# Performance work log

Measured on AMD Instinct MI355X. Metric: run time of the kernel, lower is better.

Reference implementation:

```python
import jax, jax.numpy as jnp
import numpy as np

N = 50000        # atoms
NEIGH = 12       # neighbors per atom
HID = 128
B = 500          # crystals (100 atoms each, contiguous)
NCLS = 2
BSTEPS, BMIN, BMAX = 40, 0.0, 8.0
ASTEPS, AMIN, AMAX = 10, -1.0, 1.0


def gbf(d, dmin, dmax, steps):
    # Gaussian basis expansion: exp(-(d - mu)^2 / gamma^2)
    filters = jnp.linspace(dmin, dmax, steps)
    gamma = (dmax - dmin) / steps
    return jnp.exp(-(d[..., None] - filters) ** 2 / gamma ** 2)


def sage_conv(x, W_l, b_l, W_r, dst, n):
    # PyG SAGEConv (mean aggr): out[d] = lin_l(mean_{src->d} x[src]) + lin_r(x[d])
    # lin commutes with mean, so project first (N x HID) to avoid a 600k x F gather.
    h = x @ W_l.T                                  # [N, HID]
    h_src = jnp.repeat(h, NEIGH, axis=0)           # source of edge e = e // NEIGH
    s = jax.ops.segment_sum(h_src, dst, num_segments=n)
    cnt = jax.ops.segment_sum(jnp.ones(dst.shape, h.dtype), dst, num_segments=n)
    agg = s / jnp.maximum(cnt, 1.0)[:, None]
    return agg + b_l + x @ W_r.T


def setup_inputs() -> dict:
    key = jax.random.key(0)
    ks = jax.random.split(key, 20)
    inp = {
        "bond_fea": jax.random.uniform(ks[0], (N, NEIGH), jnp.float32) * 8.0,
        "angle_fea": jax.random.uniform(ks[1], (N, NEIGH, NEIGH), jnp.float32) * 2.0 - 1.0,
        "species": jax.random.randint(ks[2], (N,), 0, 100),
        "nbr_idx": jax.random.randint(ks[3], (N, NEIGH), 0, N),
        "crys_idx": jnp.stack([jnp.arange(B) * 100, (jnp.arange(B) + 1) * 100], axis=1),
    }
    def w(k, shape):
        return jax.random.normal(k, shape, jnp.float32) * 0.05
    inp.update({
        "W1b": w(ks[4], (HID, BSTEPS * NEIGH)), "b1b": jnp.zeros((HID,), jnp.float32),
        "W1br": w(ks[5], (HID, BSTEPS * NEIGH)),
        "W1a": w(ks[6], (HID, ASTEPS * NEIGH * NEIGH)), "b1a": jnp.zeros((HID,), jnp.float32),
        "W1ar": w(ks[7], (HID, ASTEPS * NEIGH * NEIGH)),
        "W2b": w(ks[8], (HID, HID)), "b2b": jnp.zeros((HID,), jnp.float32),
        "W2br": w(ks[9], (HID, HID)),
        "W2a": w(ks[10], (HID, HID)), "b2a": jnp.zeros((HID,), jnp.float32),
        "W2ar": w(ks[11], (HID, HID)),
        "Wfc": w(ks[12], (NCLS, 2 * HID)), "bfc": jnp.zeros((NCLS,), jnp.float32),
    })
    return inp


def reference(bond_fea, angle_fea, W1b, b1b, W1br, W1a, b1a, W1ar,
              W2b, b2b, W2br, W2a, b2a, W2ar, Wfc, bfc,
              species, nbr_idx, crys_idx):
    dst = nbr_idx.reshape(-1)                               # [N*NEIGH]
    edge_fea = gbf(bond_fea, BMIN, BMAX, BSTEPS).reshape(N, -1)    # [N, 480]
    angle_f = gbf(angle_fea, AMIN, AMAX, ASTEPS).reshape(N, -1)    # [N, 1440]

    bo = jax.nn.relu(sage_conv(edge_fea, W1b, b1b, W1br, dst, N))
    ao = jax.nn.relu(sage_conv(angle_f, W1a, b1a, W1ar, dst, N))
    # dropout omitted (deterministic eval-mode reference)
    bo = jax.nn.relu(sage_conv(bo, W2b, b2b, W2br, dst, N))
    ao = jax.nn.relu(sage_conv(ao, W2a, b2a, W2ar, dst, N))

    crys_fea = jnp.concatenate([bo, ao], axis=1)            # [N, 256]
    # segment-mean pooling over contiguous [start, end) crystal ranges
    seg = jnp.searchsorted(crys_idx[:, 1], jnp.arange(N), side="right")
    cnt = (crys_idx[:, 1] - crys_idx[:, 0]).astype(crys_fea.dtype)
    pooled = jax.ops.segment_sum(crys_fea, seg, num_segments=B) / cnt[:, None]
    return pooled @ Wfc.T + bfc
```

## Files before the change

kernel.cpp:

```cpp
#include <hip/hip_runtime.h>

#define NEIGHB 12
#define HIDD 128
#define CAP 40

typedef _Float16 half8 __attribute__((ext_vector_type(8)));
typedef float f32x4 __attribute__((ext_vector_type(4)));

__global__ __launch_bounds__(256) void cvt_all(
    const float* __restrict__ W1b, const float* __restrict__ W1br, _Float16* __restrict__ O1b,
    const float* __restrict__ W1a, const float* __restrict__ W1ar, _Float16* __restrict__ O1a,
    const float* __restrict__ W2b, const float* __restrict__ W2br, _Float16* __restrict__ O2b,
    const float* __restrict__ W2a, const float* __restrict__ W2ar, _Float16* __restrict__ O2a) {
    int blk = blockIdx.x;
    const float *Wl, *Wr; _Float16* out; int K, Kp, base;
    if (blk < 512)       { Wl = W1b; Wr = W1br; out = O1b; K = 480;  Kp = 512;  base = 0; }
    else if (blk < 1984) { Wl = W1a; Wr = W1ar; out = O1a; K = 1440; Kp = 1472; base = 512; }
    else if (blk < 2112) { Wl = W2b; Wr = W2br; out = O2b; K = 128;  Kp = 128;  base = 1984; }
    else                 { Wl = W2a; Wr = W2ar; out = O2a; K = 128;  Kp = 128;  base = 2112; }
    int idx = (blk - base) * 256 + threadIdx.x;
    int n = idx / Kp, k = idx - n * Kp;
    float v = 0.f;
    if (k < K) v = (n < HIDD) ? Wl[(size_t)n * K + k] : Wr[(size_t)(n - HIDD) * K + k];
    out[idx] = (_Float16)v;
}

template <int MODE, int KTOT, int KP>
__global__ __launch_bounds__(256) void gemm_f16(
    const void* __restrict__ Ain, const _Float16* __restrict__ Wt,
    _Float16* __restrict__ Cl, _Float16* __restrict__ Cr, int rows) {
    constexpr int SUB  = (MODE == 2) ? 10 : 40;
    constexpr int RAWC = (MODE == 2) ? 144 : 12;
    constexpr float MU0 = (MODE == 2) ? -1.0f : 0.0f;
    constexpr float DMU = (MODE == 2) ? (2.0f / 9.0f) : (8.0f / 39.0f);

    __shared__ __align__(16) _Float16 As[64 * 64];
    __shared__ __align__(16) _Float16 Bs[256 * 64];

    const int tid = threadIdx.x;
    const int lane = tid & 63;
    const int wave = tid >> 6;
    const int iBase = blockIdx.x * 64;

    f32x4 acc[4][4];
#pragma unroll
    for (int a = 0; a < 4; ++a)
#pragma unroll
        for (int b = 0; b < 4; ++b)
#pragma unroll
            for (int r = 0; r < 4; ++r) acc[a][b][r] = 0.f;

    for (int kc = 0; kc < KP; kc += 64) {
        __syncthreads();
#pragma unroll
        for (int q = 0; q < 2; ++q) {
            int idx = tid + 256 * q;
            int m = idx >> 3, g = idx & 7;
            int gi = min(iBase + m, rows - 1);
            half8 v;
            if (MODE == 0) {
                v = *reinterpret_cast<const half8*>((const _Float16*)Ain + (size_t)gi * KP + kc + g * 8);
            } else {
                int k0 = kc + g * 8;
                if (k0 < KTOT) {
                    int j0 = k0 / SUB, t0 = k0 - j0 * SUB;
                    const float* rr = (const float*)Ain + (size_t)gi * RAWC;
                    float r0 = rr[j0];
                    float r1 = (MODE == 2 && t0 + 7 >= SUB) ? rr[min(j0 + 1, RAWC - 1)] : r0;
#pragma unroll
                    for (int e2 = 0; e2 < 8; ++e2) {
                        int t = t0 + e2;
                        bool c2 = (t >= SUB);
                        float d = (c2 ? r1 : r0) - (MU0 + (float)(c2 ? t - SUB : t) * DMU);
                        v[e2] = (_Float16)__expf(-25.f * d * d);
                    }
                } else {
#pragma unroll
                    for (int e2 = 0; e2 < 8; ++e2) v[e2] = (_Float16)0.f;
                }
            }
            *reinterpret_cast<half8*>(As + m * 64 + ((g ^ (m & 7)) << 3)) = v;
        }
#pragma unroll
        for (int q = 0; q < 8; ++q) {
            int idx = tid + 256 * q;
            int n = idx >> 3, g = idx & 7;
            half8 v = *reinterpret_cast<const half8*>(Wt + (size_t)n * KP + kc + g * 8);
            *reinterpret_cast<half8*>(Bs + n * 64 + ((g ^ (n & 7)) << 3)) = v;
        }
        __syncthreads();
#pragma unroll
        for (int s = 0; s < 2; ++s) {
            int cg = s * 4 + (lane >> 4);
            half8 af[4], bf[4];
#pragma unroll
            for (int a = 0; a < 4; ++a) {
                int m = a * 16 + (lane & 15);
                af[a] = *reinterpret_cast<const half8*>(As + m * 64 + ((cg ^ (m & 7)) << 3));
            }
#pragma unroll
            for (int b = 0; b < 4; ++b) {
                int n = wave * 64 + b * 16 + (lane & 15);
                bf[b] = *reinterpret_cast<const half8*>(Bs + n * 64 + ((cg ^ (n & 7)) << 3));
            }
#pragma unroll
            for (int a = 0; a < 4; ++a)
#pragma unroll
                for (int b = 0; b < 4; ++b)
                    acc[a][b] = __builtin_amdgcn_mfma_f32_16x16x32_f16(af[a], bf[b], acc[a][b], 0, 0, 0);
        }
    }

    _Float16* Cout = (wave < 2) ? Cl : Cr;
    int nBase = (wave & 1) * 64;
#pragma unroll
    for (int a = 0; a < 4; ++a) {
        int mrel = a * 16 + ((lane >> 4) << 2);
#pragma unroll
        for (int r = 0; r < 4; ++r) {
            int m = iBase + mrel + r;
            if (m < rows) {
#pragma unroll
                for (int b = 0; b < 4; ++b) {
                    int n = nBase + b * 16 + (lane & 15);
                    Cout[(size_t)m * HIDD + n] = (_Float16)acc[a][b][r];
                }
            }
        }
    }
}

__global__ void build_inc(const int* __restrict__ nbr, int* __restrict__ cnt,
                          int* __restrict__ inc, int nEdges) {
    int e = blockIdx.x * blockDim.x + threadIdx.x;
    if (e >= nEdges) return;
    int d = nbr[e];
    int src = e / NEIGHB;
    int pos = atomicAdd(&cnt[d], 1);
    if (pos < CAP) inc[(size_t)d * CAP + pos] = src;
}

__global__ __launch_bounds__(256) void agg_relu(
    const _Float16* __restrict__ Hl, const _Float16* __restrict__ Hr,
    const int* __restrict__ cnt, const int* __restrict__ inc,
    const float* __restrict__ bias, _Float16* __restrict__ O, int N) {
    int d = blockIdx.x * 16 + (threadIdx.x >> 4);
    if (d >= N) return;
    int c8 = (threadIdx.x & 15) * 8;
    int c = cnt[d];
    int cc = min(c, CAP);
    const int* lst = inc + (size_t)d * CAP;
    float s[8];
#pragma unroll
    for (int j = 0; j < 8; ++j) s[j] = 0.f;
    int e = 0;
    for (; e + 2 <= cc; e += 2) {
        int i0 = lst[e], i1 = lst[e + 1];
        half8 v0 = *reinterpret_cast<const half8*>(Hl + (size_t)i0 * HIDD + c8);
        half8 v1 = *reinterpret_cast<const half8*>(Hl + (size_t)i1 * HIDD + c8);
#pragma unroll
        for (int j = 0; j < 8; ++j) s[j] += (float)v0[j] + (float)v1[j];
    }
    if (e < cc) {
        half8 v0 = *reinterpret_cast<const half8*>(Hl + (size_t)lst[e] * HIDD + c8);
#pragma unroll
        for (int j = 0; j < 8; ++j) s[j] += (float)v0[j];
    }
    float inv = 1.f / (float)max(c, 1);
    half8 hr = *reinterpret_cast<const half8*>(Hr + (size_t)d * HIDD + c8);
    float4 b0 = *reinterpret_cast<const float4*>(bias + c8);
    float4 b1 = *reinterpret_cast<const float4*>(bias + c8 + 4);
    float bb[8] = {b0.x, b0.y, b0.z, b0.w, b1.x, b1.y, b1.z, b1.w};
    half8 o;
#pragma unroll
    for (int j = 0; j < 8; ++j)
        o[j] = (_Float16)fmaxf(s[j] * inv + bb[j] + (float)hr[j], 0.f);
    *reinterpret_cast<half8*>(O + (size_t)d * HIDD + c8) = o;
}

__global__ __launch_bounds__(256) void pool_fc(const _Float16* __restrict__ bo,
                                               const _Float16* __restrict__ ao,
                                               const int* __restrict__ crys,
                                               const float* __restrict__ Wfc,
                                               const float* __restrict__ bfc,
                                               float* __restrict__ out) {
    __shared__ float red0[256];
    __shared__ float red1[256];
    int b = blockIdx.x;
    int t = threadIdx.x;
    int s0 = crys[b * 2 + 0];
    int s1 = crys[b * 2 + 1];
    const _Float16* src = (t < HIDD) ? bo : ao;
    int col = t & (HIDD - 1);
    float s = 0.f;
    for (int i = s0; i < s1; ++i) s += (float)src[(size_t)i * HIDD + col];
    float pooled = s / (float)(s1 - s0);
    red0[t] = pooled * Wfc[t];
    red1[t] = pooled * Wfc[256 + t];
    __syncthreads();
    for (int off = 128; off >= 1; off >>= 1) {
        if (t < off) {
            red0[t] += red0[t + off];
            red1[t] += red1[t + off];
        }
        __syncthreads();
    }
    if (t == 0) {
        out[b * 2 + 0] = red0[0] + bfc[0];
        out[b * 2 + 1] = red1[0] + bfc[1];
    }
}

extern "C" void kernel_launch(void* const* d_in, const int* in_sizes, int n_in,
                              void* d_out, int out_size, void* d_ws, size_t ws_size,
                              hipStream_t stream) {
    const float* bond = (const float*)d_in[0];
    const float* angle = (const float*)d_in[1];
    const int* nbr = (const int*)d_in[3];
    const int* crys = (const int*)d_in[4];
    const float* W1b = (const float*)d_in[5];
    const float* b1b = (const float*)d_in[6];
    const float* W1br = (const float*)d_in[7];
    const float* W1a = (const float*)d_in[8];
    const float* b1a = (const float*)d_in[9];
    const float* W1ar = (const float*)d_in[10];
    const float* W2b = (const float*)d_in[11];
    const float* b2b = (const float*)d_in[12];
    const float* W2br = (const float*)d_in[13];
    const float* W2a = (const float*)d_in[14];
    const float* b2a = (const float*)d_in[15];
    const float* W2ar = (const float*)d_in[16];
    const float* Wfc = (const float*)d_in[17];
    const float* bfc = (const float*)d_in[18];
    float* out = (float*)d_out;

    const int N = in_sizes[2];
    const int B = in_sizes[4] / 2;
    const int nEdges = N * NEIGHB;

    char* p = (char*)d_ws;
    _Float16* Hl  = (_Float16*)p;  p += (size_t)N * HIDD * 2;
    _Float16* Hr  = (_Float16*)p;  p += (size_t)N * HIDD * 2;
    _Float16* bo  = (_Float16*)p;  p += (size_t)N * HIDD * 2;
    _Float16* ao  = (_Float16*)p;  p += (size_t)N * HIDD * 2;
    _Float16* bo2 = (_Float16*)p;  p += (size_t)N * HIDD * 2;
    _Float16* ao2 = (_Float16*)p;  p += (size_t)N * HIDD * 2;
    int* cnt = (int*)p;            p += (size_t)N * 4;
    int* inc = (int*)p;            p += (size_t)N * CAP * 4;
    _Float16* W1bp = (_Float16*)p; p += 256 * 512 * 2;
    _Float16* W1ap = (_Float16*)p; p += 256 * 1472 * 2;
    _Float16* W2bp = (_Float16*)p; p += 256 * 128 * 2;
    _Float16* W2ap = (_Float16*)p;

    hipMemsetAsync(cnt, 0, (size_t)N * 4, stream);
    build_inc<<<(nEdges + 255) / 256, 256, 0, stream>>>(nbr, cnt, inc, nEdges);
    cvt_all<<<2240, 256, 0, stream>>>(W1b, W1br, W1bp, W1a, W1ar, W1ap,
                                      W2b, W2br, W2bp, W2a, W2ar, W2ap);

    const int gB = (N + 63) / 64;
    const int aB = (N + 15) / 16;

    gemm_f16<1, 480, 512><<<gB, 256, 0, stream>>>(bond, W1bp, Hl, Hr, N);
    agg_relu<<<aB, 256, 0, stream>>>(Hl, Hr, cnt, inc, b1b, bo, N);
    gemm_f16<2, 1440, 1472><<<gB, 256, 0, stream>>>(angle, W1ap, Hl, Hr, N);
    agg_relu<<<aB, 256, 0, stream>>>(Hl, Hr, cnt, inc, b1a, ao, N);
    gemm_f16<0, 128, 128><<<gB, 256, 0, stream>>>(bo, W2bp, Hl, Hr, N);
    agg_relu<<<aB, 256, 0, stream>>>(Hl, Hr, cnt, inc, b2b, bo2, N);
    gemm_f16<0, 128, 128><<<gB, 256, 0, stream>>>(ao, W2ap, Hl, Hr, N);
    agg_relu<<<aB, 256, 0, stream>>>(Hl, Hr, cnt, inc, b2a, ao2, N);

    pool_fc<<<B, 256, 0, stream>>>(bo2, ao2, crys, Wfc, bfc, out);
}
```

Before: 431.3 us.

## Stage raw GBF inputs in LDS, split angle GEMM across N, widen gather unroll

For the fused Gaussian-expansion GEMMs, each block first copies its 64 rows of raw bond or angle values into shared memory with vectorized loads. The per-k-chunk expansion then reads from LDS instead of re-reading scattered global floats. The angle GEMM gains an N-split template parameter so two blocks each compute half the 256 output columns, doubling the grid. This adds parallelism but recomputes the expensive exp expansion twice per row tile. The aggregation kernel now loads four neighbor indices at once with an int4 and sums four gathered rows per iteration to raise memory-level parallelism.

```diff
diff --git a/kernel.cpp b/kernel.cpp
--- a/kernel.cpp
+++ b/kernel.cpp
@@ -25,28 +25,58 @@
     out[idx] = (_Float16)v;
 }
 
-template <int MODE, int KTOT, int KP>
+template <int MODE, int KTOT, int KP, int NS>
 __global__ __launch_bounds__(256) void gemm_f16(
     const void* __restrict__ Ain, const _Float16* __restrict__ Wt,
     _Float16* __restrict__ Cl, _Float16* __restrict__ Cr, int rows) {
     constexpr int SUB  = (MODE == 2) ? 10 : 40;
     constexpr int RAWC = (MODE == 2) ? 144 : 12;
+    constexpr int RST  = (MODE == 2) ? 148 : 12;
     constexpr float MU0 = (MODE == 2) ? -1.0f : 0.0f;
     constexpr float DMU = (MODE == 2) ? (2.0f / 9.0f) : (8.0f / 39.0f);
+    constexpr int BN = 256 / NS;
+    constexpr int NB = BN / 64;
 
     __shared__ __align__(16) _Float16 As[64 * 64];
-    __shared__ __align__(16) _Float16 Bs[256 * 64];
+    __shared__ __align__(16) _Float16 Bs[BN * 64];
+    __shared__ __align__(16) float rawS[(MODE != 0) ? 64 * RST : 4];
 
     const int tid = threadIdx.x;
     const int lane = tid & 63;
     const int wave = tid >> 6;
-    const int iBase = blockIdx.x * 64;
-
-    f32x4 acc[4][4];
+    const int nHalf = (NS == 2) ? ((int)blockIdx.x & 1) : 0;
+    const int mb = (NS == 2) ? ((int)blockIdx.x >> 1) : (int)blockIdx.x;
+    const int iBase = mb * 64;
+
+    if (MODE != 0) {
+        if (iBase + 64 <= rows) {
+            const float* gsrc = (const float*)Ain + (size_t)iBase * RAWC;
+            constexpr int NV4 = 64 * RAWC / 4;
+#pragma unroll
+            for (int q = 0; q < (NV4 + 255) / 256; ++q) {
+                int idx = tid + 256 * q;
+                if (NV4 % 256 == 0 || idx < NV4) {
+                    int r = idx / (RAWC / 4);
+                    int c4 = idx - r * (RAWC / 4);
+                    float4 v = *reinterpret_cast<const float4*>(gsrc + (size_t)idx * 4);
+                    *reinterpret_cast<float4*>(&rawS[r * RST + c4 * 4]) = v;
+                }
+            }
+        } else {
+            for (int idx = tid; idx < 64 * RAWC; idx += 256) {
+                int r = idx / RAWC, c = idx - r * RAWC;
+                int gi = iBase + r;
+                rawS[r * RST + c] = (gi < rows) ? ((const float*)Ain)[(size_t)gi * RAWC + c] : 0.f;
+            }
+        }
+        __syncthreads();
+    }
+
+    f32x4 acc[4][NB];
 #pragma unroll
     for (int a = 0; a < 4; ++a)
 #pragma unroll
-        for (int b = 0; b < 4; ++b)
+        for (int b = 0; b < NB; ++b)
 #pragma unroll
             for (int r = 0; r < 4; ++r) acc[a][b][r] = 0.f;
 
@@ -56,17 +86,16 @@
         for (int q = 0; q < 2; ++q) {
             int idx = tid + 256 * q;
             int m = idx >> 3, g = idx & 7;
-            int gi = min(iBase + m, rows - 1);
             half8 v;
             if (MODE == 0) {
+                int gi = min(iBase + m, rows - 1);
                 v = *reinterpret_cast<const half8*>((const _Float16*)Ain + (size_t)gi * KP + kc + g * 8);
             } else {
                 int k0 = kc + g * 8;
                 if (k0 < KTOT) {
                     int j0 = k0 / SUB, t0 = k0 - j0 * SUB;
-                    const float* rr = (const float*)Ain + (size_t)gi * RAWC;
-                    float r0 = rr[j0];
-                    float r1 = (MODE == 2 && t0 + 7 >= SUB) ? rr[min(j0 + 1, RAWC - 1)] : r0;
+                    float r0 = rawS[m * RST + j0];
+                    float r1 = (MODE == 2 && t0 + 7 >= SUB) ? rawS[m * RST + j0 + 1] : r0;
 #pragma unroll
                     for (int e2 = 0; e2 < 8; ++e2) {
                         int t = t0 + e2;
@@ -82,37 +111,36 @@
             *reinterpret_cast<half8*>(As + m * 64 + ((g ^ (m & 7)) << 3)) = v;
         }
 #pragma unroll
-        for (int q = 0; q < 8; ++q) {
+        for (int q = 0; q < BN / 32; ++q) {
             int idx = tid + 256 * q;
             int n = idx >> 3, g = idx & 7;
-            half8 v = *reinterpret_cast<const half8*>(Wt + (size_t)n * KP + kc + g * 8);
+            half8 v = *reinterpret_cast<const half8*>(
+                Wt + (size_t)(nHalf * BN + n) * KP + kc + g * 8);
             *reinterpret_cast<half8*>(Bs + n * 64 + ((g ^ (n & 7)) << 3)) = v;
         }
         __syncthreads();
 #pragma unroll
         for (int s = 0; s < 2; ++s) {
             int cg = s * 4 + (lane >> 4);
-            half8 af[4], bf[4];
+            half8 af[4], bf[NB];
 #pragma unroll
             for (int a = 0; a < 4; ++a) {
                 int m = a * 16 + (lane & 15);
                 af[a] = *reinterpret_cast<const half8*>(As + m * 64 + ((cg ^ (m & 7)) << 3));
             }
 #pragma unroll
-            for (int b = 0; b < 4; ++b) {
-                int n = wave * 64 + b * 16 + (lane & 15);
+            for (int b = 0; b < NB; ++b) {
+                int n = wave * (16 * NB) + b * 16 + (lane & 15);
                 bf[b] = *reinterpret_cast<const half8*>(Bs + n * 64 + ((cg ^ (n & 7)) << 3));
             }
 #pragma unroll
             for (int a = 0; a < 4; ++a)
 #pragma unroll
-                for (int b = 0; b < 4; ++b)
+                for (int b = 0; b < NB; ++b)
                     acc[a][b] = __builtin_amdgcn_mfma_f32_16x16x32_f16(af[a], bf[b], acc[a][b], 0, 0, 0);
         }
     }
 
-    _Float16* Cout = (wave < 2) ? Cl : Cr;
-    int nBase = (wave & 1) * 64;
 #pragma unroll
     for (int a = 0; a < 4; ++a) {
         int mrel = a * 16 + ((lane >> 4) << 2);
@@ -121,9 +149,10 @@
             int m = iBase + mrel + r;
             if (m < rows) {
 #pragma unroll
-                for (int b = 0; b < 4; ++b) {
-                    int n = nBase + b * 16 + (lane & 15);
-                    Cout[(size_t)m * HIDD + n] = (_Float16)acc[a][b][r];
+                for (int b = 0; b < NB; ++b) {
+                    int gcol = nHalf * BN + wave * (16 * NB) + b * 16 + (lane & 15);
+                    _Float16* Cout = (gcol < HIDD) ? Cl : Cr;
+                    Cout[(size_t)m * HIDD + (gcol & (HIDD - 1))] = (_Float16)acc[a][b][r];
                 }
             }
         }
@@ -150,26 +179,29 @@
     int c = cnt[d];
     int cc = min(c, CAP);
     const int* lst = inc + (size_t)d * CAP;
-    float s[8];
-#pragma unroll
-    for (int j = 0; j < 8; ++j) s[j] = 0.f;
-    int e = 0;
-    for (; e + 2 <= cc; e += 2) {
-        int i0 = lst[e], i1 = lst[e + 1];
-        half8 v0 = *reinterpret_cast<const half8*>(Hl + (size_t)i0 * HIDD + c8);
-        half8 v1 = *reinterpret_cast<const half8*>(Hl + (size_t)i1 * HIDD + c8);
-#pragma unroll
-        for (int j = 0; j < 8; ++j) s[j] += (float)v0[j] + (float)v1[j];
-    }
-    if (e < cc) {
-        half8 v0 = *reinterpret_cast<const half8*>(Hl + (size_t)lst[e] * HIDD + c8);
-#pragma unroll
-        for (int j = 0; j < 8; ++j) s[j] += (float)v0[j];
-    }
-    float inv = 1.f / (float)max(c, 1);
     half8 hr = *reinterpret_cast<const half8*>(Hr + (size_t)d * HIDD + c8);
     float4 b0 = *reinterpret_cast<const float4*>(bias + c8);
     float4 b1 = *reinterpret_cast<const float4*>(bias + c8 + 4);
+    float s[8];
+#pragma unroll
+    for (int j = 0; j < 8; ++j) s[j] = 0.f;
+    int e = 0;
+    for (; e + 4 <= cc; e += 4) {
+        int4 ii = *reinterpret_cast<const int4*>(lst + e);
+        half8 v0 = *reinterpret_cast<const half8*>(Hl + (size_t)ii.x * HIDD + c8);
+        half8 v1 = *reinterpret_cast<const half8*>(Hl + (size_t)ii.y * HIDD + c8);
+        half8 v2 = *reinterpret_cast<const half8*>(Hl + (size_t)ii.z * HIDD + c8);
+        half8 v3 = *reinterpret_cast<const half8*>(Hl + (size_t)ii.w * HIDD + c8);
+#pragma unroll
+        for (int j = 0; j < 8; ++j)
+            s[j] += ((float)v0[j] + (float)v1[j]) + ((float)v2[j] + (float)v3[j]);
+    }
+    for (; e < cc; ++e) {
+        half8 v0 = *reinterpret_cast<const half8*>(Hl + (size_t)lst[e] * HIDD + c8);
+#pragma unroll
+        for (int j = 0; j < 8; ++j) s[j] += (float)v0[j];
+    }
+    float inv = 1.f / (float)max(c, 1);
     float bb[8] = {b0.x, b0.y, b0.z, b0.w, b1.x, b1.y, b1.z, b1.w};
     half8 o;
 #pragma unroll
@@ -260,13 +292,13 @@
     const int gB = (N + 63) / 64;
     const int aB = (N + 15) / 16;
 
-    gemm_f16<1, 480, 512><<<gB, 256, 0, stream>>>(bond, W1bp, Hl, Hr, N);
+    gemm_f16<1, 480, 512, 1><<<gB, 256, 0, stream>>>(bond, W1bp, Hl, Hr, N);
     agg_relu<<<aB, 256, 0, stream>>>(Hl, Hr, cnt, inc, b1b, bo, N);
-    gemm_f16<2, 1440, 1472><<<gB, 256, 0, stream>>>(angle, W1ap, Hl, Hr, N);
+    gemm_f16<2, 1440, 1472, 2><<<gB * 2, 256, 0, stream>>>(angle, W1ap, Hl, Hr, N);
     agg_relu<<<aB, 256, 0, stream>>>(Hl, Hr, cnt, inc, b1a, ao, N);
-    gemm_f16<0, 128, 128><<<gB, 256, 0, stream>>>(bo, W2bp, Hl, Hr, N);
+    gemm_f16<0, 128, 128, 1><<<gB, 256, 0, stream>>>(bo, W2bp, Hl, Hr, N);
     agg_relu<<<aB, 256, 0, stream>>>(Hl, Hr, cnt, inc, b2b, bo2, N);
-    gemm_f16<0, 128, 128><<<gB, 256, 0, stream>>>(ao, W2ap, Hl, Hr, N);
+    gemm_f16<0, 128, 128, 1><<<gB, 256, 0, stream>>>(ao, W2ap, Hl, Hr, N);
     agg_relu<<<aB, 256, 0, stream>>>(Hl, Hr, cnt, inc, b2a, ao2, N);
 
     pool_fc<<<B, 256, 0, stream>>>(bo2, ao2, crys, Wfc, bfc, out);
```

New measurement: 450.1 us. 4.4% more time.

## Register-prefetch next K tile in GEMM and fuse bond/angle aggregation kernels

Applied to the files above, without the earlier changes.

The GEMM now prefetches the next K-chunk's weights and raw features into registers while MFMAs run on the current tile, and computes the Gaussian expansion after the compute. This hides global-load latency behind math. Bond and angle branches also get separate H buffers, so one agg2 kernel aggregates both per layer. That halves the aggregation launches and shares the index loads, with the first 12 neighbors fetched unconditionally to expose memory-level parallelism. The cost is higher register pressure, which may reduce occupancy.

```diff
diff --git a/kernel.cpp b/kernel.cpp
--- a/kernel.cpp
+++ b/kernel.cpp
@@ -33,6 +33,7 @@
     constexpr int RAWC = (MODE == 2) ? 144 : 12;
     constexpr float MU0 = (MODE == 2) ? -1.0f : 0.0f;
     constexpr float DMU = (MODE == 2) ? (2.0f / 9.0f) : (8.0f / 39.0f);
+    constexpr int NT = KP / 64;
 
     __shared__ __align__(16) _Float16 As[64 * 64];
     __shared__ __align__(16) _Float16 Bs[256 * 64];
@@ -41,6 +42,72 @@
     const int lane = tid & 63;
     const int wave = tid >> 6;
     const int iBase = blockIdx.x * 64;
+    const int mrow = tid >> 3;
+    const int g = tid & 7;
+    const int g8 = g * 8;
+
+    const int gi0 = min(iBase + mrow, rows - 1);
+    const int gi1 = min(iBase + mrow + 32, rows - 1);
+    const _Float16* Ap = (const _Float16*)Ain;
+    const float* rr0 = (const float*)Ain + (size_t)gi0 * RAWC;
+    const float* rr1 = (const float*)Ain + (size_t)gi1 * RAWC;
+
+    half8 bReg[8];
+    half8 aExp[2];
+    float r0v[2], r1v[2];
+
+#define PREFETCH(KC)                                                              \
+    {                                                                             \
+        _Pragma("unroll")                                                         \
+        for (int q = 0; q < 8; ++q)                                               \
+            bReg[q] = *reinterpret_cast<const half8*>(                            \
+                Wt + (size_t)(mrow + 32 * q) * KP + (KC) + g8);                   \
+        if (MODE == 0) {                                                          \
+            aExp[0] = *reinterpret_cast<const half8*>(Ap + (size_t)gi0 * KP + (KC) + g8); \
+            aExp[1] = *reinterpret_cast<const half8*>(Ap + (size_t)gi1 * KP + (KC) + g8); \
+        } else {                                                                  \
+            int k0 = (KC) + g8;                                                   \
+            if (k0 < KTOT) {                                                      \
+                int j0 = k0 / SUB;                                                \
+                r0v[0] = rr0[j0]; r0v[1] = rr1[j0];                               \
+                if (MODE == 2) {                                                  \
+                    int jn = min(j0 + 1, RAWC - 1);                               \
+                    r1v[0] = rr0[jn]; r1v[1] = rr1[jn];                           \
+                }                                                                 \
+            }                                                                     \
+        }                                                                         \
+    }
+
+#define EXPAND(KC)                                                                \
+    if (MODE != 0) {                                                              \
+        int k0 = (KC) + g8;                                                       \
+        if (k0 < KTOT) {                                                          \
+            int j0 = k0 / SUB, t0 = k0 - j0 * SUB;                                \
+            _Pragma("unroll")                                                     \
+            for (int q = 0; q < 2; ++q) {                                         \
+                float ra = r0v[q];                                                \
+                float rb = (MODE == 2) ? r1v[q] : r0v[q];                         \
+                half8 v;                                                          \
+                _Pragma("unroll")                                                 \
+                for (int e2 = 0; e2 < 8; ++e2) {                                  \
+                    int tt = t0 + e2;                                             \
+                    bool c2 = (tt >= SUB);                                        \
+                    float dd = (c2 ? rb : ra) -                                   \
+                               (MU0 + (float)(c2 ? tt - SUB : tt) * DMU);         \
+                    v[e2] = (_Float16)__expf(-25.f * dd * dd);                    \
+                }                                                                 \
+                aExp[q] = v;                                                      \
+            }                                                                     \
+        } else {                                                                  \
+            _Pragma("unroll")                                                     \
+            for (int q = 0; q < 2; ++q) {                                         \
+                half8 v;                                                          \
+                _Pragma("unroll")                                                 \
+                for (int e2 = 0; e2 < 8; ++e2) v[e2] = (_Float16)0.f;             \
+                aExp[q] = v;                                                      \
+            }                                                                     \
+        }                                                                         \
+    }
 
     f32x4 acc[4][4];
 #pragma unroll
@@ -50,45 +117,26 @@
 #pragma unroll
             for (int r = 0; r < 4; ++r) acc[a][b][r] = 0.f;
 
-    for (int kc = 0; kc < KP; kc += 64) {
+    PREFETCH(0);
+    EXPAND(0);
+
+#pragma unroll 1
+    for (int t = 0; t < NT; ++t) {
+        const int kc = t * 64;
         __syncthreads();
 #pragma unroll
         for (int q = 0; q < 2; ++q) {
-            int idx = tid + 256 * q;
-            int m = idx >> 3, g = idx & 7;
-            int gi = min(iBase + m, rows - 1);
-            half8 v;
-            if (MODE == 0) {
-                v = *reinterpret_cast<const half8*>((const _Float16*)Ain + (size_t)gi * KP + kc + g * 8);
-            } else {
-                int k0 = kc + g * 8;
-                if (k0 < KTOT) {
-                    int j0 = k0 / SUB, t0 = k0 - j0 * SUB;
-                    const float* rr = (const float*)Ain + (size_t)gi * RAWC;
-                    float r0 = rr[j0];
-                    float r1 = (MODE == 2 && t0 + 7 >= SUB) ? rr[min(j0 + 1, RAWC - 1)] : r0;
-#pragma unroll
-                    for (int e2 = 0; e2 < 8; ++e2) {
-                        int t = t0 + e2;
-                        bool c2 = (t >= SUB);
-                        float d = (c2 ? r1 : r0) - (MU0 + (float)(c2 ? t - SUB : t) * DMU);
-                        v[e2] = (_Float16)__expf(-25.f * d * d);
-                    }
-                } else {
-#pragma unroll
-                    for (int e2 = 0; e2 < 8; ++e2) v[e2] = (_Float16)0.f;
-                }
-            }
-            *reinterpret_cast<half8*>(As + m * 64 + ((g ^ (m & 7)) << 3)) = v;
+            int m = mrow + 32 * q;
+            *reinterpret_cast<half8*>(As + m * 64 + ((g ^ (m & 7)) << 3)) = aExp[q];
         }
 #pragma unroll
         for (int q = 0; q < 8; ++q) {
-            int idx = tid + 256 * q;
-            int n = idx >> 3, g = idx & 7;
-            half8 v = *reinterpret_cast<const half8*>(Wt + (size_t)n * KP + kc + g * 8);
-            *reinterpret_cast<half8*>(Bs + n * 64 + ((g ^ (n & 7)) << 3)) = v;
+            int n = mrow + 32 * q;
+            *reinterpret_cast<half8*>(Bs + n * 64 + ((g ^ (n & 7)) << 3)) = bReg[q];
         }
         __syncthreads();
+        const bool hasNext = (t + 1) < NT;
+        if (hasNext) PREFETCH(kc + 64);
 #pragma unroll
         for (int s = 0; s < 2; ++s) {
             int cg = s * 4 + (lane >> 4);
@@ -109,7 +157,10 @@
                 for (int b = 0; b < 4; ++b)
                     acc[a][b] = __builtin_amdgcn_mfma_f32_16x16x32_f16(af[a], bf[b], acc[a][b], 0, 0, 0);
         }
-    }
+        if (hasNext) EXPAND(kc + 64);
+    }
+#undef PREFETCH
+#undef EXPAND
 
     _Float16* Cout = (wave < 2) ? Cl : Cr;
     int nBase = (wave & 1) * 64;
@@ -140,42 +191,66 @@
     if (pos < CAP) inc[(size_t)d * CAP + pos] = src;
 }
 
-__global__ __launch_bounds__(256) void agg_relu(
-    const _Float16* __restrict__ Hl, const _Float16* __restrict__ Hr,
+__global__ __launch_bounds__(256) void agg2(
+    const _Float16* __restrict__ Hbl, const _Float16* __restrict__ Hbr,
+    const _Float16* __restrict__ Hal, const _Float16* __restrict__ Har,
     const int* __restrict__ cnt, const int* __restrict__ inc,
-    const float* __restrict__ bias, _Float16* __restrict__ O, int N) {
+    const float* __restrict__ biasB, const float* __restrict__ biasA,
+    _Float16* __restrict__ Ob, _Float16* __restrict__ Oa, int N) {
     int d = blockIdx.x * 16 + (threadIdx.x >> 4);
     if (d >= N) return;
     int c8 = (threadIdx.x & 15) * 8;
     int c = cnt[d];
     int cc = min(c, CAP);
     const int* lst = inc + (size_t)d * CAP;
-    float s[8];
-#pragma unroll
-    for (int j = 0; j < 8; ++j) s[j] = 0.f;
-    int e = 0;
-    for (; e + 2 <= cc; e += 2) {
-        int i0 = lst[e], i1 = lst[e + 1];
-        half8 v0 = *reinterpret_cast<const half8*>(Hl + (size_t)i0 * HIDD + c8);
-        half8 v1 = *reinterpret_cast<const half8*>(Hl + (size_t)i1 * HIDD + c8);
-#pragma unroll
-        for (int j = 0; j < 8; ++j) s[j] += (float)v0[j] + (float)v1[j];
-    }
-    if (e < cc) {
-        half8 v0 = *reinterpret_cast<const half8*>(Hl + (size_t)lst[e] * HIDD + c8);
-#pragma unroll
-        for (int j = 0; j < 8; ++j) s[j] += (float)v0[j];
+    int4 q0 = *reinterpret_cast<const int4*>(lst);
+    int4 q1 = *reinterpret_cast<const int4*>(lst + 4);
+    int4 q2 = *reinterpret_cast<const int4*>(lst + 8);
+    int idx[12] = {q0.x, q0.y, q0.z, q0.w, q1.x, q1.y, q1.z, q1.w,
+                   q2.x, q2.y, q2.z, q2.w};
+    half8 vb[12], va[12];
+#pragma unroll
+    for (int e = 0; e < 12; ++e) {
+        int ii = (e < cc) ? idx[e] : 0;
+        vb[e] = *reinterpret_cast<const half8*>(Hbl + (size_t)ii * HIDD + c8);
+        va[e] = *reinterpret_cast<const half8*>(Hal + (size_t)ii * HIDD + c8);
+    }
+    float sb[8], sa[8];
+#pragma unroll
+    for (int j = 0; j < 8; ++j) { sb[j] = 0.f; sa[j] = 0.f; }
+#pragma unroll
+    for (int e = 0; e < 12; ++e) {
+        float w = (e < cc) ? 1.f : 0.f;
+#pragma unroll
+        for (int j = 0; j < 8; ++j) {
+            sb[j] = fmaf(w, (float)vb[e][j], sb[j]);
+            sa[j] = fmaf(w, (float)va[e][j], sa[j]);
+        }
+    }
+    for (int e = 12; e < cc; ++e) {
+        int ii = lst[e];
+        half8 xb = *reinterpret_cast<const half8*>(Hbl + (size_t)ii * HIDD + c8);
+        half8 xa = *reinterpret_cast<const half8*>(Hal + (size_t)ii * HIDD + c8);
+#pragma unroll
+        for (int j = 0; j < 8; ++j) { sb[j] += (float)xb[j]; sa[j] += (float)xa[j]; }
     }
     float inv = 1.f / (float)max(c, 1);
-    half8 hr = *reinterpret_cast<const half8*>(Hr + (size_t)d * HIDD + c8);
-    float4 b0 = *reinterpret_cast<const float4*>(bias + c8);
-    float4 b1 = *reinterpret_cast<const float4*>(bias + c8 + 4);
-    float bb[8] = {b0.x, b0.y, b0.z, b0.w, b1.x, b1.y, b1.z, b1.w};
-    half8 o;
-#pragma unroll
-    for (int j = 0; j < 8; ++j)
-        o[j] = (_Float16)fmaxf(s[j] * inv + bb[j] + (float)hr[j], 0.f);
-    *reinterpret_cast<half8*>(O + (size_t)d * HIDD + c8) = o;
+    half8 rb = *reinterpret_cast<const half8*>(Hbr + (size_t)d * HIDD + c8);
+    half8 ra = *reinterpret_cast<const half8*>(Har + (size_t)d * HIDD + c8);
+    float4 bb0 = *reinterpret_cast<const float4*>(biasB + c8);
+    float4 bb1 = *reinterpret_cast<const float4*>(biasB + c8 + 4);
+    float4 ba0 = *reinterpret_cast<const float4*>(biasA + c8);
+    float4 ba1 = *reinterpret_cast<const float4*>(biasA + c8 + 4);
+    float fb[8] = {bb0.x, bb0.y, bb0.z, bb0.w, bb1.x, bb1.y, bb1.z, bb1.w};
+    float fa[8] = {ba0.x, ba0.y, ba0.z, ba0.w, ba1.x, ba1.y, ba1.z, ba1.w};
+    half8 ob, oa;
+#pragma unroll
+    for (int j = 0; j < 8; ++j) {
+        ob[j] = (_Float16)fmaxf(sb[j] * inv + fb[j] + (float)rb[j], 0.f);
+        oa[j] = (_Float16)fmaxf(sa[j] * inv + fa[j] + (float)ra[j], 0.f);
+    }
+    *reinterpret_cast<half8*>(Ob + (size_t)d * HIDD + c8) = ob;
+    *reinterpret_cast<half8*>(Oa + (size_t)d * HIDD + c8) = oa;
 }
 
 __global__ __launch_bounds__(256) void pool_fc(const _Float16* __restrict__ bo,
@@ -239,8 +314,10 @@
     const int nEdges = N * NEIGHB;
 
     char* p = (char*)d_ws;
-    _Float16* Hl  = (_Float16*)p;  p += (size_t)N * HIDD * 2;
-    _Float16* Hr  = (_Float16*)p;  p += (size_t)N * HIDD * 2;
+    _Float16* Hbl = (_Float16*)p;  p += (size_t)N * HIDD * 2;
+    _Float16* Hbr = (_Float16*)p;  p += (size_t)N * HIDD * 2;
+    _Float16* Hal = (_Float16*)p;  p += (size_t)N * HIDD * 2;
+    _Float16* Har = (_Float16*)p;  p += (size_t)N * HIDD * 2;
     _Float16* bo  = (_Float16*)p;  p += (size_t)N * HIDD * 2;
     _Float16* ao  = (_Float16*)p;  p += (size_t)N * HIDD * 2;
     _Float16* bo2 = (_Float16*)p;  p += (size_t)N * HIDD * 2;
@@ -260,14 +337,12 @@
     const int gB = (N + 63) / 64;
     const int aB = (N + 15) / 16;
 
-    gemm_f16<1, 480, 512><<<gB, 256, 0, stream>>>(bond, W1bp, Hl, Hr, N);
-    agg_relu<<<aB, 256, 0, stream>>>(Hl, Hr, cnt, inc, b1b, bo, N);
-    gemm_f16<2, 1440, 1472><<<gB, 256, 0, stream>>>(angle, W1ap, Hl, Hr, N);
-    agg_relu<<<aB, 256, 0, stream>>>(Hl, Hr, cnt, inc, b1a, ao, N);
-    gemm_f16<0, 128, 128><<<gB, 256, 0, stream>>>(bo, W2bp, Hl, Hr, N);
-    agg_relu<<<aB, 256, 0, stream>>>(Hl, Hr, cnt, inc, b2b, bo2, N);
-    gemm_f16<0, 128, 128><<<gB, 256, 0, stream>>>(ao, W2ap, Hl, Hr, N);
-    agg_relu<<<aB, 256, 0, stream>>>(Hl, Hr, cnt, inc, b2a, ao2, N);
+    gemm_f16<1, 480, 512><<<gB, 256, 0, stream>>>(bond, W1bp, Hbl, Hbr, N);
+    gemm_f16<2, 1440, 1472><<<gB, 256, 0, stream>>>(angle, W1ap, Hal, Har, N);
+    agg2<<<aB, 256, 0, stream>>>(Hbl, Hbr, Hal, Har, cnt, inc, b1b, b1a, bo, ao, N);
+    gemm_f16<0, 128, 128><<<gB, 256, 0, stream>>>(bo, W2bp, Hbl, Hbr, N);
+    gemm_f16<0, 128, 128><<<gB, 256, 0, stream>>>(ao, W2ap, Hal, Har, N);
+    agg2<<<aB, 256, 0, stream>>>(Hbl, Hbr, Hal, Har, cnt, inc, b2b, b2a, bo2, ao2, N);
 
     pool_fc<<<B, 256, 0, stream>>>(bo2, ao2, crys, Wfc, bfc, out);
 }
```

After: 411.4 us. -4.6%, faster.
